# Kernel optimization log

Measured on AMD Instinct MI355X. Metric: run time of the kernel, lower is better.

## Reference

```python
import jax, jax.numpy as jnp
import numpy as np


def _norm_cdf(x):
    # standard normal CDF via erf
    return 0.5 * (1.0 + jax.lax.erf(x * np.float32(1.0 / np.sqrt(2.0))))


def setup_inputs() -> dict:
    key = jax.random.key(0)
    k1, k2 = jax.random.split(key)
    shape = (8192, 4096)
    y_pred = jax.random.normal(k1, shape, dtype=jnp.float32)
    y_true = jax.random.normal(k2, shape, dtype=jnp.float32)
    sigma_v, sigma_u = 1.0, 0.5
    log_std_v = jnp.asarray(np.log(sigma_v), dtype=jnp.float32)
    log_std_u = jnp.asarray(np.log(sigma_u), dtype=jnp.float32)
    return {"y_pred": y_pred, "y_true": y_true,
            "log_std_v": log_std_v, "log_std_u": log_std_u}


def reference(y_pred, y_true, log_std_v, log_std_u):
    std_v = jnp.exp(log_std_v)
    std_u = jnp.exp(log_std_u)
    sigma2 = std_v ** 2 + std_u ** 2
    sigma = jnp.sqrt(sigma2)
    llamda = jnp.sqrt(std_u ** 2 / std_v ** 2)
    resid = y_true - y_pred
    # torch code detaches before the CDF (numpy round-trip) -> stop_gradient
    cdf_arg = jax.lax.stop_gradient(-llamda * resid / sigma)
    ff = _norm_cdf(cdf_arg)
    log_likelihood = (-0.5 * jnp.log(jnp.float32(np.pi / 2.0))
                      - 0.5 * jnp.log(sigma2)
                      + jnp.log(ff)
                      - resid ** 2 / (2.0 * sigma2))
    return -jnp.mean(log_likelihood)
```

## Files before the change

### kernel.cpp

```cpp
#include <hip/hip_runtime.h>
#include <math.h>


__device__ __forceinline__ float ll_elem(float r, float karg, float nk2, float inv2s2) {
    float r2 = r * r;
    float x  = karg * r;
    float ax = fabsf(x);
    float t  = __builtin_amdgcn_rcpf(fmaf(0.3275911f, ax, 1.0f));
    float p  = fmaf(t, 1.061405429f, -1.453152027f);
    p = fmaf(t, p, 1.421413741f);
    p = fmaf(t, p, -0.284496736f);
    p = fmaf(t, p, 0.254829592f);
    p *= t;
    float e  = __expf(nk2 * r2);
    float ea = fmaf(-p, e, 1.0f);
    float ev = copysignf(ea, x);
    return __logf(fmaf(0.5f, ev, 0.5f)) - r2 * inv2s2;
}

__global__ __launch_bounds__(256) void gnll_stage1(
    const float4* __restrict__ yp, const float4* __restrict__ yt,
    const float* __restrict__ lsv, const float* __restrict__ lsu,
    float* __restrict__ partials, int n4)
{
    const float std_v  = __expf(lsv[0]);
    const float std_u  = __expf(lsu[0]);
    const float sigma2 = std_v * std_v + std_u * std_u;
    const float sigma  = sqrtf(sigma2);
    const float llamda = std_u / std_v;
    const float karg   = -llamda / sigma * 0.70710678118654752f;
    const float nk2    = -karg * karg;
    const float c0     = -0.5f * logf(1.57079632679489662f)
                         - 0.5f * logf(sigma2);
    const float inv2s2 = 0.5f / sigma2;

    float acc = 0.0f;
    int   cnt = 0;
    const int tid = blockIdx.x * blockDim.x + threadIdx.x;
    const int nth = gridDim.x * blockDim.x;

    float4 pA0, pA1, pA2, pA3, tA0, tA1, tA2, tA3;
    float4 pB0, pB1, pB2, pB3, tB0, tB1, tB2, tB3;

#define LOAD_A(g) { int b_ = (g) * nth * 4 + tid;                                   \
    pA0 = yp[b_]; pA1 = yp[b_ + nth]; pA2 = yp[b_ + 2*nth]; pA3 = yp[b_ + 3*nth];   \
    tA0 = yt[b_]; tA1 = yt[b_ + nth]; tA2 = yt[b_ + 2*nth]; tA3 = yt[b_ + 3*nth]; }
#define LOAD_B(g) { int b_ = (g) * nth * 4 + tid;                                   \
    pB0 = yp[b_]; pB1 = yp[b_ + nth]; pB2 = yp[b_ + 2*nth]; pB3 = yp[b_ + 3*nth];   \
    tB0 = yt[b_]; tB1 = yt[b_ + nth]; tB2 = yt[b_ + 2*nth]; tB3 = yt[b_ + 3*nth]; }
#define COMP1(P, T) { float s_ =                                                    \
      ll_elem(T.x - P.x, karg, nk2, inv2s2) + ll_elem(T.y - P.y, karg, nk2, inv2s2) \
    + ll_elem(T.z - P.z, karg, nk2, inv2s2) + ll_elem(T.w - P.w, karg, nk2, inv2s2);\
    acc += s_; }
#define COMP_A { COMP1(pA0, tA0) COMP1(pA1, tA1) COMP1(pA2, tA2) COMP1(pA3, tA3) cnt += 16; }
#define COMP_B { COMP1(pB0, tB0) COMP1(pB1, tB1) COMP1(pB2, tB2) COMP1(pB3, tB3) cnt += 16; }

    const int ngroups = n4 / (nth * 4);
    if (ngroups > 0) {
        LOAD_A(0)
        int g = 0;
        for (; g + 2 < ngroups; g += 2) {
            LOAD_B(g + 1)
            COMP_A
            LOAD_A(g + 2)
            COMP_B
        }
        if (g + 1 < ngroups) {
            LOAD_B(g + 1)
            COMP_A
            COMP_B
        } else {
            COMP_A
        }
    }

    for (int i = ngroups * nth * 4 + tid; i < n4; i += nth) {
        float4 p = yp[i];
        float4 t = yt[i];
        acc += ll_elem(t.x - p.x, karg, nk2, inv2s2)
             + ll_elem(t.y - p.y, karg, nk2, inv2s2)
             + ll_elem(t.z - p.z, karg, nk2, inv2s2)
             + ll_elem(t.w - p.w, karg, nk2, inv2s2);
        cnt += 4;
    }

    acc = fmaf((float)cnt, c0, acc);

    #pragma unroll
    for (int off = 32; off > 0; off >>= 1)
        acc += __shfl_down(acc, off, 64);

    __shared__ float ws[4];
    int lane = threadIdx.x & 63;
    int wid  = threadIdx.x >> 6;
    if (lane == 0) ws[wid] = acc;
    __syncthreads();
    if (threadIdx.x == 0)
        partials[blockIdx.x] = (ws[0] + ws[1]) + (ws[2] + ws[3]);
}

__global__ __launch_bounds__(256) void gnll_stage2(
    const float* __restrict__ partials, float* __restrict__ out,
    int nparts, float neg_inv_n)
{
    float acc = 0.0f;
    for (int i = threadIdx.x; i < nparts; i += 256)
        acc += partials[i];

    #pragma unroll
    for (int off = 32; off > 0; off >>= 1)
        acc += __shfl_down(acc, off, 64);

    __shared__ float ws[4];
    int lane = threadIdx.x & 63;
    int wid  = threadIdx.x >> 6;
    if (lane == 0) ws[wid] = acc;
    __syncthreads();
    if (threadIdx.x == 0)
        out[0] = ((ws[0] + ws[1]) + (ws[2] + ws[3])) * neg_inv_n;
}

extern "C" void kernel_launch(void* const* d_in, const int* in_sizes, int n_in,
                              void* d_out, int out_size, void* d_ws, size_t ws_size,
                              hipStream_t stream) {
    const float4* yp = (const float4*)d_in[0];
    const float4* yt = (const float4*)d_in[1];
    const float* lsv = (const float*)d_in[2];
    const float* lsu = (const float*)d_in[3];
    float* out = (float*)d_out;
    float* partials = (float*)d_ws;

    long long n = (long long)in_sizes[0];
    int n4 = (int)(n / 4);
    float neg_inv_n = -1.0f / (float)n;

    const int block = 256;
    const int grid  = 2048;
    gnll_stage1<<<grid, block, 0, stream>>>(yp, yt, lsv, lsu, partials, n4);
    gnll_stage2<<<1, block, 0, stream>>>(partials, out, grid, neg_inv_n);
}
```

Before: 52.84 us.

## Hand-schedule global loads with inline asm and explicit vmcnt waits

For the exact problem size (four groups per thread), the stage-1 loop is replaced by fully unrolled code. It issues global_load_dwordx4 through inline asm and uses partial s_waitcnt vmcnt with sched barriers, so two groups of loads stay in flight while the previous group is computed. The aim is more memory-level parallelism and tighter overlap of loads with the erf/log math than the compiler-scheduled double buffering gave. In exchange the code depends on one specific shape, falls back to a simple loop otherwise, and bypasses compiler scheduling, which is fragile (e.g. waitcnt counting across inline asm).

```diff
diff --git a/kernel.cpp b/kernel.cpp
--- a/kernel.cpp
+++ b/kernel.cpp
@@ -1,6 +1,15 @@
 #include <hip/hip_runtime.h>
 #include <math.h>
 
+
+typedef float f32x4 __attribute__((ext_vector_type(4)));
+
+#define GLOAD(dst, addr) \
+    asm volatile("global_load_dwordx4 %0, %1, off" : "=v"(dst) : "v"(addr) : "memory")
+
+#define VMWAIT(n) do { \
+    asm volatile("s_waitcnt vmcnt(" #n ")" ::: "memory"); \
+    __builtin_amdgcn_sched_barrier(0); } while (0)
 
 __device__ __forceinline__ float ll_elem(float r, float karg, float nk2, float inv2s2) {
     float r2 = r * r;
@@ -34,57 +43,57 @@
                          - 0.5f * logf(sigma2);
     const float inv2s2 = 0.5f / sigma2;
 
-    float acc = 0.0f;
-    int   cnt = 0;
     const int tid = blockIdx.x * blockDim.x + threadIdx.x;
     const int nth = gridDim.x * blockDim.x;
 
-    float4 pA0, pA1, pA2, pA3, tA0, tA1, tA2, tA3;
-    float4 pB0, pB1, pB2, pB3, tB0, tB1, tB2, tB3;
+    float acc = 0.0f;
 
-#define LOAD_A(g) { int b_ = (g) * nth * 4 + tid;                                   \
-    pA0 = yp[b_]; pA1 = yp[b_ + nth]; pA2 = yp[b_ + 2*nth]; pA3 = yp[b_ + 3*nth];   \
-    tA0 = yt[b_]; tA1 = yt[b_ + nth]; tA2 = yt[b_ + 2*nth]; tA3 = yt[b_ + 3*nth]; }
-#define LOAD_B(g) { int b_ = (g) * nth * 4 + tid;                                   \
-    pB0 = yp[b_]; pB1 = yp[b_ + nth]; pB2 = yp[b_ + 2*nth]; pB3 = yp[b_ + 3*nth];   \
-    tB0 = yt[b_]; tB1 = yt[b_ + nth]; tB2 = yt[b_ + 2*nth]; tB3 = yt[b_ + 3*nth]; }
-#define COMP1(P, T) { float s_ =                                                    \
-      ll_elem(T.x - P.x, karg, nk2, inv2s2) + ll_elem(T.y - P.y, karg, nk2, inv2s2) \
-    + ll_elem(T.z - P.z, karg, nk2, inv2s2) + ll_elem(T.w - P.w, karg, nk2, inv2s2);\
-    acc += s_; }
-#define COMP_A { COMP1(pA0, tA0) COMP1(pA1, tA1) COMP1(pA2, tA2) COMP1(pA3, tA3) cnt += 16; }
-#define COMP_B { COMP1(pB0, tB0) COMP1(pB1, tB1) COMP1(pB2, tB2) COMP1(pB3, tB3) cnt += 16; }
+#define LOADG(P0,P1,P2,P3,T0,T1,T2,T3, g) { \
+    const float4* bp_ = yp + (size_t)(g) * nth * 4 + tid; \
+    const float4* bt_ = yt + (size_t)(g) * nth * 4 + tid; \
+    GLOAD(P0, bp_);            GLOAD(T0, bt_); \
+    GLOAD(P1, bp_ + nth);      GLOAD(T1, bt_ + nth); \
+    GLOAD(P2, bp_ + 2 * nth);  GLOAD(T2, bt_ + 2 * nth); \
+    GLOAD(P3, bp_ + 3 * nth);  GLOAD(T3, bt_ + 3 * nth); }
+
+#define COMP1(P, T) { \
+    acc += ll_elem(T.x - P.x, karg, nk2, inv2s2) + ll_elem(T.y - P.y, karg, nk2, inv2s2) \
+         + ll_elem(T.z - P.z, karg, nk2, inv2s2) + ll_elem(T.w - P.w, karg, nk2, inv2s2); }
+
+#define COMPG(P0,P1,P2,P3,T0,T1,T2,T3) { \
+    COMP1(P0, T0) COMP1(P1, T1) COMP1(P2, T2) COMP1(P3, T3) }
 
     const int ngroups = n4 / (nth * 4);
-    if (ngroups > 0) {
-        LOAD_A(0)
-        int g = 0;
-        for (; g + 2 < ngroups; g += 2) {
-            LOAD_B(g + 1)
-            COMP_A
-            LOAD_A(g + 2)
-            COMP_B
+    if (ngroups == 4 && n4 == nth * 16) {
+        f32x4 pa0, pa1, pa2, pa3, ta0, ta1, ta2, ta3;
+        f32x4 pb0, pb1, pb2, pb3, tb0, tb1, tb2, tb3;
+
+        LOADG(pa0,pa1,pa2,pa3, ta0,ta1,ta2,ta3, 0)
+        LOADG(pb0,pb1,pb2,pb3, tb0,tb1,tb2,tb3, 1)
+        VMWAIT(8);
+        COMPG(pa0,pa1,pa2,pa3, ta0,ta1,ta2,ta3)
+        LOADG(pa0,pa1,pa2,pa3, ta0,ta1,ta2,ta3, 2)
+        VMWAIT(8);
+        COMPG(pb0,pb1,pb2,pb3, tb0,tb1,tb2,tb3)
+        LOADG(pb0,pb1,pb2,pb3, tb0,tb1,tb2,tb3, 3)
+        VMWAIT(8);
+        COMPG(pa0,pa1,pa2,pa3, ta0,ta1,ta2,ta3)
+        VMWAIT(0);
+        COMPG(pb0,pb1,pb2,pb3, tb0,tb1,tb2,tb3)
+        acc += 64.0f * c0;
+    } else {
+        int cnt = 0;
+        for (int i = tid; i < n4; i += nth) {
+            float4 p = yp[i];
+            float4 t = yt[i];
+            acc += ll_elem(t.x - p.x, karg, nk2, inv2s2)
+                 + ll_elem(t.y - p.y, karg, nk2, inv2s2)
+                 + ll_elem(t.z - p.z, karg, nk2, inv2s2)
+                 + ll_elem(t.w - p.w, karg, nk2, inv2s2);
+            cnt += 4;
         }
-        if (g + 1 < ngroups) {
-            LOAD_B(g + 1)
-            COMP_A
-            COMP_B
-        } else {
-            COMP_A
-        }
+        acc = fmaf((float)cnt, c0, acc);
     }
-
-    for (int i = ngroups * nth * 4 + tid; i < n4; i += nth) {
-        float4 p = yp[i];
-        float4 t = yt[i];
-        acc += ll_elem(t.x - p.x, karg, nk2, inv2s2)
-             + ll_elem(t.y - p.y, karg, nk2, inv2s2)
-             + ll_elem(t.z - p.z, karg, nk2, inv2s2)
-             + ll_elem(t.w - p.w, karg, nk2, inv2s2);
-        cnt += 4;
-    }
-
-    acc = fmaf((float)cnt, c0, acc);
 
     #pragma unroll
     for (int off = 32; off > 0; off >>= 1)
```

After: 55.77 us. 1.06x slower.
